# Kernel optimization log

Measured on AMD Instinct MI355X. Metric: run time of the kernel, lower is better.

The kernel has to match this reference:

```python
import jax, jax.numpy as jnp
import numpy as np
from jax.ops import segment_sum

N_NODES = 10000
N_EDGES = 160000
IN_FEAT = 256
OUT_FEAT = 256
NUM_RELS = 16


def setup_inputs() -> dict:
    key = jax.random.key(0)
    ks = jax.random.split(key, 8)
    feat = jax.random.normal(ks[0], (N_NODES, IN_FEAT), dtype=jnp.float32)
    Wf = jax.random.normal(ks[1], (NUM_RELS, IN_FEAT, OUT_FEAT), dtype=jnp.float32)
    Wb = jax.random.normal(ks[2], (NUM_RELS, IN_FEAT, OUT_FEAT), dtype=jnp.float32)
    loop_weight = jax.random.normal(ks[3], (IN_FEAT, OUT_FEAT), dtype=jnp.float32)
    forward_bias = jnp.zeros((OUT_FEAT,), dtype=jnp.float32)
    backward_bias = jnp.zeros((OUT_FEAT,), dtype=jnp.float32)
    self_bias = jnp.zeros((OUT_FEAT,), dtype=jnp.float32)
    src = jax.random.randint(ks[4], (N_EDGES,), 0, N_NODES, dtype=jnp.int32)
    dst = jax.random.randint(ks[5], (N_EDGES,), 0, N_NODES, dtype=jnp.int32)
    etypes = jax.random.randint(ks[6], (N_EDGES,), 0, NUM_RELS, dtype=jnp.int32)
    return {
        "feat": feat, "Wf": Wf, "Wb": Wb, "loop_weight": loop_weight,
        "forward_bias": forward_bias, "backward_bias": backward_bias,
        "self_bias": self_bias, "src": src, "dst": dst, "etypes": etypes,
        "use_dis_weight": 0, "drop_out": 0,
    }


def _inv_degree(idx, n):
    # dgl.norm_by_dst: 1/in-degree, with inf (zero-degree) replaced by 0
    deg = segment_sum(jnp.ones(idx.shape[0], dtype=jnp.float32), idx, num_segments=n)
    return jnp.where(deg > 0, 1.0 / deg, 0.0)


def _typed_pass(feat, W, bias, src_idx, dst_idx, etypes, norm_per_edge, n):
    # Per-relation projection of all nodes (grouped GEMM as R dense GEMMs),
    # then gather per-edge by (etype, src) -- avoids [E,in,out] weight gather.
    proj = jnp.einsum('ni,rio->rno', feat, W)          # [R, N, out]
    m = proj[etypes, src_idx] + bias                   # [E, out]
    m = m * norm_per_edge[:, None]
    return segment_sum(m, dst_idx, num_segments=n)     # [N, out]


def reference(feat, Wf, Wb, loop_weight, forward_bias, backward_bias,
              self_bias, src, dst, etypes, use_dis_weight, drop_out):
    n = feat.shape[0]
    # forward graph: messages src -> dst, norm by dst in-degree
    norm_f = _inv_degree(dst, n)[dst]                  # [E]
    m_forward = _typed_pass(feat, Wf, forward_bias, src, dst, etypes, norm_f, n)
    # reversed graph: src'=dst, dst'=src, same etype; norm by reversed dst in-degree
    norm_b = _inv_degree(src, n)[src]                  # [E]
    m_backward = _typed_pass(feat, Wb, backward_bias, dst, src, etypes, norm_b, n)
    # self loop (drop_out=False); faithful quirk: s += s + self_bias -> 2s + bias
    s = feat @ loop_weight
    s = s + s + self_bias
    return s + m_forward + m_backward
```

## Files before the change

kernel.cpp:

```cpp
#include <hip/hip_runtime.h>
#include <hip/hip_bf16.h>
#include <stdint.h>

#define N_NODES 10000
#define N_EDGES 160000
#define FEAT    256
#define NRELS   16
#define BM      64
#define NCHUNK  32
#define GRIDX   40
#define KBYTES  512

typedef __attribute__((ext_vector_type(8))) short bf16x8;
typedef __attribute__((ext_vector_type(4))) float f32x4;

__device__ __forceinline__ unsigned short f2bf(float f) {
    union { float f; unsigned u; } v; v.f = f;
    unsigned u = v.u;
    u += 0x7FFFu + ((u >> 16) & 1u);
    return (unsigned short)(u >> 16);
}
__device__ __forceinline__ float bf2f(unsigned short u) {
    union { unsigned u; float f; } v; v.u = ((unsigned)u) << 16;
    return v.f;
}

__global__ __launch_bounds__(256) void k_prep(const float4* __restrict__ src4,
                                              ushort4* __restrict__ dst4, int n4,
                                              const int* __restrict__ src,
                                              const int* __restrict__ dst,
                                              int* degd, int* degs) {
    int i = blockIdx.x * 256 + threadIdx.x;
    if (i < n4) {
        float4 v = src4[i];
        ushort4 r;
        r.x = f2bf(v.x); r.y = f2bf(v.y); r.z = f2bf(v.z); r.w = f2bf(v.w);
        dst4[i] = r;
    }
    if (i < N_EDGES) {
        atomicAdd(&degd[dst[i]], 1);
        atomicAdd(&degs[src[i]], 1);
    }
}

__global__ __launch_bounds__(256) void k_wtall(const float* __restrict__ Wf,
                                               const float* __restrict__ Wb,
                                               const float* __restrict__ lw,
                                               unsigned short* __restrict__ wall,
                                               unsigned short* __restrict__ lwt) {
    __shared__ float tile[64][65];
    int z = blockIdx.z;
    const float* w;
    unsigned short* o;
    if (z < 16)      { w = Wf + (size_t)z * 65536;        o = wall + (size_t)(z * 2) * 65536; }
    else if (z < 32) { w = Wb + (size_t)(z - 16) * 65536; o = wall + (size_t)((z - 16) * 2 + 1) * 65536; }
    else             { w = lw;                            o = lwt; }
    int i0 = blockIdx.x * 64, o0 = blockIdx.y * 64;
    int t = threadIdx.x;
    int c = t & 63, q = t >> 6;
#pragma unroll
    for (int it = 0; it < 16; it++) {
        int i = it * 4 + q;
        tile[i][c] = w[(size_t)(i0 + i) * 256 + o0 + c];
    }
    __syncthreads();
#pragma unroll
    for (int it = 0; it < 16; it++) {
        int oo = it * 4 + q;
        o[(size_t)(o0 + oo) * 256 + i0 + c] = f2bf(tile[c][oo]);
    }
}

__global__ __launch_bounds__(1024) void k_scan(const int* __restrict__ degd,
                                               const int* __restrict__ degs,
                                               int* offf, int* offb,
                                               int* curf, int* curb,
                                               float* normf, float* normb) {
    __shared__ int sf[1024], sb[1024];
    int t = threadIdx.x;
    const int CH = (N_NODES + 1023) / 1024;
    int base = t * CH;
    int sumf = 0, sumb = 0;
    for (int i = 0; i < CH; i++) {
        int n = base + i;
        if (n < N_NODES) { sumf += degd[n]; sumb += degs[n]; }
    }
    sf[t] = sumf; sb[t] = sumb;
    __syncthreads();
    for (int d = 1; d < 1024; d <<= 1) {
        int vf = (t >= d) ? sf[t - d] : 0;
        int vb = (t >= d) ? sb[t - d] : 0;
        __syncthreads();
        sf[t] += vf; sb[t] += vb;
        __syncthreads();
    }
    int runf = t ? sf[t - 1] : 0;
    int runb = t ? sb[t - 1] : 0;
    for (int i = 0; i < CH; i++) {
        int n = base + i;
        if (n < N_NODES) {
            int df = degd[n], db = degs[n];
            offf[n] = runf; offb[n] = runb;
            curf[n] = runf; curb[n] = runb;
            normf[n] = df > 0 ? 1.f / (float)df : 0.f;
            normb[n] = db > 0 ? 1.f / (float)db : 0.f;
            runf += df; runb += db;
        }
    }
    if (t == 1023) { offf[N_NODES] = runf; offb[N_NODES] = runb; }
}

__global__ __launch_bounds__(256) void k_fill(const int* __restrict__ et,
                                              const int* __restrict__ src,
                                              const int* __restrict__ dst,
                                              int* curf, int* curb,
                                              int* csrf, int* csrb) {
    int e = blockIdx.x * 256 + threadIdx.x;
    if (e < N_EDGES) {
        int s = src[e], d = dst[e], r = et[e];
        csrf[atomicAdd(&curf[d], 1)] = (r * 2) * N_NODES + s;
        csrb[atomicAdd(&curb[s], 1)] = (r * 2 + 1) * N_NODES + d;
    }
}

__global__ __launch_bounds__(256) void k_proj(const unsigned short* __restrict__ featb,
                                              const unsigned short* __restrict__ wall,
                                              const unsigned short* __restrict__ lwt,
                                              const float* __restrict__ sbias,
                                              unsigned short* __restrict__ proj,
                                              float* __restrict__ out) {
    __shared__ __align__(16) char lds[BM * KBYTES];
    int rd = blockIdx.x;
    if (rd > NCHUNK) return;
    int m0 = blockIdx.y * BM;
    int t = threadIdx.x;
    int wave = t >> 6, lane = t & 63;
    int nb = wave * 64, lr = lane & 15, lg = lane >> 4;
    bool self = (rd == NCHUNK);
    const unsigned short* wr = self ? lwt : wall + (size_t)rd * 256 * FEAT;

    {
        int rl = t >> 5;
        int kb = (t & 31) << 4;
#pragma unroll
        for (int it = 0; it < 8; it++) {
            int row = it * 8 + rl;
            int gr = m0 + row; if (gr > N_NODES - 1) gr = N_NODES - 1;
            bf16x8 v = *(const bf16x8*)(featb + gr * FEAT + (kb >> 1));
            *(bf16x8*)(lds + row * KBYTES + (kb ^ ((row & 7) << 4))) = v;
        }
    }
    __syncthreads();

    f32x4 acc[4][4] = {};
    bf16x8 bcur[4], bnxt[4];
#pragma unroll
    for (int ni = 0; ni < 4; ni++)
        bcur[ni] = *(const bf16x8*)(wr + (nb + ni * 16 + lr) * FEAT + lg * 8);
#pragma unroll
    for (int k0 = 0; k0 < FEAT; k0 += 32) {
        if (k0 + 32 < FEAT) {
#pragma unroll
            for (int ni = 0; ni < 4; ni++)
                bnxt[ni] = *(const bf16x8*)(wr + (nb + ni * 16 + lr) * FEAT + k0 + 32 + lg * 8);
        }
        int kb = (k0 + lg * 8) * 2;
        bf16x8 a[4];
#pragma unroll
        for (int mi = 0; mi < 4; mi++) {
            int row = mi * 16 + lr;
            a[mi] = *(const bf16x8*)(lds + row * KBYTES + (kb ^ ((row & 7) << 4)));
        }
#pragma unroll
        for (int mi = 0; mi < 4; mi++)
#pragma unroll
            for (int ni = 0; ni < 4; ni++)
                acc[mi][ni] = __builtin_amdgcn_mfma_f32_16x16x32_bf16(a[mi], bcur[ni], acc[mi][ni], 0, 0, 0);
#pragma unroll
        for (int ni = 0; ni < 4; ni++) bcur[ni] = bnxt[ni];
    }

    if (self) {
        for (int mi = 0; mi < 4; mi++) {
#pragma unroll
            for (int j = 0; j < 4; j++) {
                int row = m0 + mi * 16 + lg * 4 + j;
                if (row < N_NODES) {
                    for (int ni = 0; ni < 4; ni++) {
                        int col = nb + ni * 16 + lr;
                        out[(size_t)row * FEAT + col] = 2.0f * acc[mi][ni][j] + sbias[col];
                    }
                }
            }
        }
        return;
    }

    __syncthreads();
    for (int mi = 0; mi < 4; mi++) {
#pragma unroll
        for (int j = 0; j < 4; j++) {
            int row = mi * 16 + lg * 4 + j;
            int sw = (row & 7) << 4;
            for (int ni = 0; ni < 4; ni++) {
                int cb = (nb + ni * 16 + lr) * 2;
                *(unsigned short*)(lds + row * KBYTES + (cb ^ sw)) = f2bf(acc[mi][ni][j]);
            }
        }
    }
    __syncthreads();

    {
        int rl = t >> 5;
        int kb = (t & 31) << 4;
#pragma unroll
        for (int it = 0; it < 8; it++) {
            int row = it * 8 + rl;
            int gr = m0 + row;
            if (gr < N_NODES)
                *(bf16x8*)(proj + ((size_t)rd * N_NODES + gr) * FEAT + (kb >> 1)) =
                    *(const bf16x8*)(lds + row * KBYTES + (kb ^ ((row & 7) << 4)));
        }
    }
}

__global__ __launch_bounds__(256) void k_reduce(const unsigned short* __restrict__ proj,
                                                const int* __restrict__ csrf,
                                                const int* __restrict__ csrb,
                                                const int* __restrict__ offf,
                                                const int* __restrict__ offb,
                                                const float* __restrict__ normf,
                                                const float* __restrict__ normb,
                                                const float* __restrict__ biasf,
                                                const float* __restrict__ biasb,
                                                float* __restrict__ out) {
    int node = blockIdx.x * 4 + (threadIdx.x >> 6);
    if (node >= N_NODES) return;
    int lane = threadIdx.x & 63;
    int half = lane >> 5;
    int li = lane & 31;

    float af[8] = {0,0,0,0,0,0,0,0};
    float ab[8] = {0,0,0,0,0,0,0,0};

    int b0 = offf[node], b1 = offf[node + 1];
#pragma unroll 4
    for (int s = b0 + half; s < b1; s += 2) {
        int c = csrf[s];
        bf16x8 m = *(const bf16x8*)(proj + (size_t)c * FEAT + li * 8);
#pragma unroll
        for (int k = 0; k < 8; k++) af[k] += bf2f((unsigned short)m[k]);
    }
    int c0 = offb[node], c1 = offb[node + 1];
#pragma unroll 4
    for (int s = c0 + half; s < c1; s += 2) {
        int c = csrb[s];
        bf16x8 m = *(const bf16x8*)(proj + (size_t)c * FEAT + li * 8);
#pragma unroll
        for (int k = 0; k < 8; k++) ab[k] += bf2f((unsigned short)m[k]);
    }

    float nf = normf[node], nbv = normb[node];
    float v[8];
#pragma unroll
    for (int k = 0; k < 8; k++) v[k] = nf * af[k] + nbv * ab[k];
#pragma unroll
    for (int k = 0; k < 8; k++) v[k] += __shfl_xor(v[k], 32);

    int col = li * 8 + half * 4;
    float4 bfv = *(const float4*)(biasf + col);
    float4 bbv = *(const float4*)(biasb + col);
    float fb = (b1 > b0) ? 1.f : 0.f;
    float bb = (c1 > c0) ? 1.f : 0.f;
    float4 o = *(float4*)(out + (size_t)node * FEAT + col);
    int k0 = half * 4;
    o.x += v[k0 + 0] + fb * bfv.x + bb * bbv.x;
    o.y += v[k0 + 1] + fb * bfv.y + bb * bbv.y;
    o.z += v[k0 + 2] + fb * bfv.z + bb * bbv.z;
    o.w += v[k0 + 3] + fb * bfv.w + bb * bbv.w;
    *(float4*)(out + (size_t)node * FEAT + col) = o;
}

extern "C" void kernel_launch(void* const* d_in, const int* in_sizes, int n_in,
                              void* d_out, int out_size, void* d_ws, size_t ws_size,
                              hipStream_t stream) {
    const float* feat  = (const float*)d_in[0];
    const float* Wf    = (const float*)d_in[1];
    const float* Wb    = (const float*)d_in[2];
    const float* lw    = (const float*)d_in[3];
    const float* fbias = (const float*)d_in[4];
    const float* bbias = (const float*)d_in[5];
    const float* sbias = (const float*)d_in[6];
    const int*   src   = (const int*)d_in[7];
    const int*   dst   = (const int*)d_in[8];
    const int*   et    = (const int*)d_in[9];
    float* out = (float*)d_out;

    char* ws = (char*)d_ws;
    size_t off = 0;
    auto alloc = [&](size_t bytes) { void* p = ws + off; off = (off + bytes + 255) & ~(size_t)255; return p; };

    int*   degd  = (int*)alloc(N_NODES * 4);
    int*   degs  = (int*)alloc(N_NODES * 4);
    size_t zero_bytes = off;
    int*   offf  = (int*)alloc((N_NODES + 1) * 4);
    int*   offb  = (int*)alloc((N_NODES + 1) * 4);
    int*   curf  = (int*)alloc(N_NODES * 4);
    int*   curb  = (int*)alloc(N_NODES * 4);
    float* normf = (float*)alloc(N_NODES * 4);
    float* normb = (float*)alloc(N_NODES * 4);
    int*   csrf  = (int*)alloc(N_EDGES * 4);
    int*   csrb  = (int*)alloc(N_EDGES * 4);
    unsigned short* featb = (unsigned short*)alloc((size_t)N_NODES * FEAT * 2);
    unsigned short* wall  = (unsigned short*)alloc((size_t)NCHUNK * 256 * FEAT * 2);
    unsigned short* lwt   = (unsigned short*)alloc((size_t)FEAT * FEAT * 2);
    unsigned short* proj  = (unsigned short*)alloc((size_t)NCHUNK * N_NODES * FEAT * 2);
    (void)ws_size;

    hipMemsetAsync(d_ws, 0, zero_bytes, stream);

    {
        int n4 = N_NODES * FEAT / 4;
        k_prep<<<(n4 + 255) / 256, 256, 0, stream>>>((const float4*)feat, (ushort4*)featb, n4,
                                                     src, dst, degd, degs);
    }
    {
        dim3 gw(4, 4, 33);
        k_wtall<<<gw, 256, 0, stream>>>(Wf, Wb, lw, wall, lwt);
    }
    k_scan<<<1, 1024, 0, stream>>>(degd, degs, offf, offb, curf, curb, normf, normb);
    k_fill<<<(N_EDGES + 255) / 256, 256, 0, stream>>>(et, src, dst, curf, curb, csrf, csrb);

    {
        dim3 grid(GRIDX, (N_NODES + BM - 1) / BM);
        k_proj<<<grid, 256, 0, stream>>>(featb, wall, lwt, sbias, proj, out);
    }

    k_reduce<<<(N_NODES + 3) / 4, 256, 0, stream>>>(proj, csrf, csrb, offf, offb,
                                                    normf, normb, fbias, bbias, out);
}
```

Measured before the change: 225.7 us.

## Replace single-block scan with atomic block offsets, move self-loop into reduce

Replaces the single-block 1024-thread prefix scan with a multi-block kernel that gets per-block base offsets from global atomics. CSR segments stay contiguous per node but are no longer ordered by node id. The self-loop projection now goes through the same bf16 projection path as a 33rd slab, so k_reduce writes out directly instead of doing a read-modify-write of fp32 out. The LDS swizzle pattern for the epilogue store is also changed to cut bank conflicts. The costs are an extra bf16 rounding on the self-loop term and an extra 5 MB projection slab that k_reduce must read.

```diff
diff --git a/kernel.cpp b/kernel.cpp
--- a/kernel.cpp
+++ b/kernel.cpp
@@ -7,7 +7,7 @@
 #define FEAT    256
 #define NRELS   16
 #define BM      64
-#define NCHUNK  32
+#define NPROJ   33
 #define GRIDX   40
 #define KBYTES  512
 
@@ -46,15 +46,14 @@
 __global__ __launch_bounds__(256) void k_wtall(const float* __restrict__ Wf,
                                                const float* __restrict__ Wb,
                                                const float* __restrict__ lw,
-                                               unsigned short* __restrict__ wall,
-                                               unsigned short* __restrict__ lwt) {
+                                               unsigned short* __restrict__ wall) {
     __shared__ float tile[64][65];
     int z = blockIdx.z;
     const float* w;
     unsigned short* o;
     if (z < 16)      { w = Wf + (size_t)z * 65536;        o = wall + (size_t)(z * 2) * 65536; }
     else if (z < 32) { w = Wb + (size_t)(z - 16) * 65536; o = wall + (size_t)((z - 16) * 2 + 1) * 65536; }
-    else             { w = lw;                            o = lwt; }
+    else             { w = lw;                            o = wall + (size_t)32 * 65536; }
     int i0 = blockIdx.x * 64, o0 = blockIdx.y * 64;
     int t = threadIdx.x;
     int c = t & 63, q = t >> 6;
@@ -71,43 +70,40 @@
     }
 }
 
-__global__ __launch_bounds__(1024) void k_scan(const int* __restrict__ degd,
-                                               const int* __restrict__ degs,
-                                               int* offf, int* offb,
-                                               int* curf, int* curb,
-                                               float* normf, float* normb) {
-    __shared__ int sf[1024], sb[1024];
+__global__ __launch_bounds__(256) void k_off(const int* __restrict__ degd,
+                                             const int* __restrict__ degs,
+                                             int* offf, int* offb,
+                                             int* curf, int* curb,
+                                             float* normf, float* normb,
+                                             int* gcnt) {
+    __shared__ int sf[256], sb[256];
+    __shared__ int basef, baseb;
     int t = threadIdx.x;
-    const int CH = (N_NODES + 1023) / 1024;
-    int base = t * CH;
-    int sumf = 0, sumb = 0;
-    for (int i = 0; i < CH; i++) {
-        int n = base + i;
-        if (n < N_NODES) { sumf += degd[n]; sumb += degs[n]; }
-    }
-    sf[t] = sumf; sb[t] = sumb;
-    __syncthreads();
-    for (int d = 1; d < 1024; d <<= 1) {
+    int n = blockIdx.x * 256 + t;
+    int df = (n < N_NODES) ? degd[n] : 0;
+    int db = (n < N_NODES) ? degs[n] : 0;
+    sf[t] = df; sb[t] = db;
+    __syncthreads();
+    for (int d = 1; d < 256; d <<= 1) {
         int vf = (t >= d) ? sf[t - d] : 0;
         int vb = (t >= d) ? sb[t - d] : 0;
         __syncthreads();
         sf[t] += vf; sb[t] += vb;
         __syncthreads();
     }
-    int runf = t ? sf[t - 1] : 0;
-    int runb = t ? sb[t - 1] : 0;
-    for (int i = 0; i < CH; i++) {
-        int n = base + i;
-        if (n < N_NODES) {
-            int df = degd[n], db = degs[n];
-            offf[n] = runf; offb[n] = runb;
-            curf[n] = runf; curb[n] = runb;
-            normf[n] = df > 0 ? 1.f / (float)df : 0.f;
-            normb[n] = db > 0 ? 1.f / (float)db : 0.f;
-            runf += df; runb += db;
-        }
-    }
-    if (t == 1023) { offf[N_NODES] = runf; offb[N_NODES] = runb; }
+    if (t == 255) {
+        basef = atomicAdd(&gcnt[0], sf[255]);
+        baseb = atomicAdd(&gcnt[1], sb[255]);
+    }
+    __syncthreads();
+    if (n < N_NODES) {
+        int ef = basef + sf[t] - df;
+        int eb = baseb + sb[t] - db;
+        offf[n] = ef; offb[n] = eb;
+        curf[n] = ef; curb[n] = eb;
+        normf[n] = df > 0 ? 1.f / (float)df : 0.f;
+        normb[n] = db > 0 ? 1.f / (float)db : 0.f;
+    }
 }
 
 __global__ __launch_bounds__(256) void k_fill(const int* __restrict__ et,
@@ -125,19 +121,15 @@
 
 __global__ __launch_bounds__(256) void k_proj(const unsigned short* __restrict__ featb,
                                               const unsigned short* __restrict__ wall,
-                                              const unsigned short* __restrict__ lwt,
-                                              const float* __restrict__ sbias,
-                                              unsigned short* __restrict__ proj,
-                                              float* __restrict__ out) {
+                                              unsigned short* __restrict__ proj) {
     __shared__ __align__(16) char lds[BM * KBYTES];
     int rd = blockIdx.x;
-    if (rd > NCHUNK) return;
+    if (rd >= NPROJ) return;
     int m0 = blockIdx.y * BM;
     int t = threadIdx.x;
     int wave = t >> 6, lane = t & 63;
     int nb = wave * 64, lr = lane & 15, lg = lane >> 4;
-    bool self = (rd == NCHUNK);
-    const unsigned short* wr = self ? lwt : wall + (size_t)rd * 256 * FEAT;
+    const unsigned short* wr = wall + (size_t)rd * 256 * FEAT;
 
     {
         int rl = t >> 5;
@@ -180,28 +172,12 @@
         for (int ni = 0; ni < 4; ni++) bcur[ni] = bnxt[ni];
     }
 
-    if (self) {
-        for (int mi = 0; mi < 4; mi++) {
-#pragma unroll
-            for (int j = 0; j < 4; j++) {
-                int row = m0 + mi * 16 + lg * 4 + j;
-                if (row < N_NODES) {
-                    for (int ni = 0; ni < 4; ni++) {
-                        int col = nb + ni * 16 + lr;
-                        out[(size_t)row * FEAT + col] = 2.0f * acc[mi][ni][j] + sbias[col];
-                    }
-                }
-            }
-        }
-        return;
-    }
-
     __syncthreads();
     for (int mi = 0; mi < 4; mi++) {
 #pragma unroll
         for (int j = 0; j < 4; j++) {
             int row = mi * 16 + lg * 4 + j;
-            int sw = (row & 7) << 4;
+            int sw = ((row >> 2) & 3) << 5;
             for (int ni = 0; ni < 4; ni++) {
                 int cb = (nb + ni * 16 + lr) * 2;
                 *(unsigned short*)(lds + row * KBYTES + (cb ^ sw)) = f2bf(acc[mi][ni][j]);
@@ -219,7 +195,7 @@
             int gr = m0 + row;
             if (gr < N_NODES)
                 *(bf16x8*)(proj + ((size_t)rd * N_NODES + gr) * FEAT + (kb >> 1)) =
-                    *(const bf16x8*)(lds + row * KBYTES + (kb ^ ((row & 7) << 4)));
+                    *(const bf16x8*)(lds + row * KBYTES + (kb ^ (((row >> 2) & 3) << 5)));
         }
     }
 }
@@ -229,10 +205,13 @@
                                                 const int* __restrict__ csrb,
                                                 const int* __restrict__ offf,
                                                 const int* __restrict__ offb,
+                                                const int* __restrict__ degd,
+                                                const int* __restrict__ degs,
                                                 const float* __restrict__ normf,
                                                 const float* __restrict__ normb,
                                                 const float* __restrict__ biasf,
                                                 const float* __restrict__ biasb,
+                                                const float* __restrict__ sbias,
                                                 float* __restrict__ out) {
     int node = blockIdx.x * 4 + (threadIdx.x >> 6);
     if (node >= N_NODES) return;
@@ -243,7 +222,8 @@
     float af[8] = {0,0,0,0,0,0,0,0};
     float ab[8] = {0,0,0,0,0,0,0,0};
 
-    int b0 = offf[node], b1 = offf[node + 1];
+    int b0 = offf[node], dfc = degd[node];
+    int b1 = b0 + dfc;
 #pragma unroll 4
     for (int s = b0 + half; s < b1; s += 2) {
         int c = csrf[s];
@@ -251,7 +231,8 @@
 #pragma unroll
         for (int k = 0; k < 8; k++) af[k] += bf2f((unsigned short)m[k]);
     }
-    int c0 = offb[node], c1 = offb[node + 1];
+    int c0 = offb[node], dbc = degs[node];
+    int c1 = c0 + dbc;
 #pragma unroll 4
     for (int s = c0 + half; s < c1; s += 2) {
         int c = csrb[s];
@@ -267,17 +248,20 @@
 #pragma unroll
     for (int k = 0; k < 8; k++) v[k] += __shfl_xor(v[k], 32);
 
+    bf16x8 sf = *(const bf16x8*)(proj + ((size_t)32 * N_NODES + node) * FEAT + li * 8);
+
     int col = li * 8 + half * 4;
     float4 bfv = *(const float4*)(biasf + col);
     float4 bbv = *(const float4*)(biasb + col);
-    float fb = (b1 > b0) ? 1.f : 0.f;
-    float bb = (c1 > c0) ? 1.f : 0.f;
-    float4 o = *(float4*)(out + (size_t)node * FEAT + col);
+    float4 sbv = *(const float4*)(sbias + col);
+    float fb = (dfc > 0) ? 1.f : 0.f;
+    float bb = (dbc > 0) ? 1.f : 0.f;
     int k0 = half * 4;
-    o.x += v[k0 + 0] + fb * bfv.x + bb * bbv.x;
-    o.y += v[k0 + 1] + fb * bfv.y + bb * bbv.y;
-    o.z += v[k0 + 2] + fb * bfv.z + bb * bbv.z;
-    o.w += v[k0 + 3] + fb * bfv.w + bb * bbv.w;
+    float4 o;
+    o.x = v[k0 + 0] + 2.f * bf2f((unsigned short)sf[k0 + 0]) + sbv.x + fb * bfv.x + bb * bbv.x;
+    o.y = v[k0 + 1] + 2.f * bf2f((unsigned short)sf[k0 + 1]) + sbv.y + fb * bfv.y + bb * bbv.y;
+    o.z = v[k0 + 2] + 2.f * bf2f((unsigned short)sf[k0 + 2]) + sbv.z + fb * bfv.z + bb * bbv.z;
+    o.w = v[k0 + 3] + 2.f * bf2f((unsigned short)sf[k0 + 3]) + sbv.w + fb * bfv.w + bb * bbv.w;
     *(float4*)(out + (size_t)node * FEAT + col) = o;
 }
 
@@ -302,9 +286,10 @@
 
     int*   degd  = (int*)alloc(N_NODES * 4);
     int*   degs  = (int*)alloc(N_NODES * 4);
+    int*   gcnt  = (int*)alloc(64);
     size_t zero_bytes = off;
-    int*   offf  = (int*)alloc((N_NODES + 1) * 4);
-    int*   offb  = (int*)alloc((N_NODES + 1) * 4);
+    int*   offf  = (int*)alloc(N_NODES * 4);
+    int*   offb  = (int*)alloc(N_NODES * 4);
     int*   curf  = (int*)alloc(N_NODES * 4);
     int*   curb  = (int*)alloc(N_NODES * 4);
     float* normf = (float*)alloc(N_NODES * 4);
@@ -312,9 +297,8 @@
     int*   csrf  = (int*)alloc(N_EDGES * 4);
     int*   csrb  = (int*)alloc(N_EDGES * 4);
     unsigned short* featb = (unsigned short*)alloc((size_t)N_NODES * FEAT * 2);
-    unsigned short* wall  = (unsigned short*)alloc((size_t)NCHUNK * 256 * FEAT * 2);
-    unsigned short* lwt   = (unsigned short*)alloc((size_t)FEAT * FEAT * 2);
-    unsigned short* proj  = (unsigned short*)alloc((size_t)NCHUNK * N_NODES * FEAT * 2);
+    unsigned short* wall  = (unsigned short*)alloc((size_t)NPROJ * 256 * FEAT * 2);
+    unsigned short* proj  = (unsigned short*)alloc((size_t)NPROJ * N_NODES * FEAT * 2);
     (void)ws_size;
 
     hipMemsetAsync(d_ws, 0, zero_bytes, stream);
@@ -326,16 +310,18 @@
     }
     {
         dim3 gw(4, 4, 33);
-        k_wtall<<<gw, 256, 0, stream>>>(Wf, Wb, lw, wall, lwt);
-    }
-    k_scan<<<1, 1024, 0, stream>>>(degd, degs, offf, offb, curf, curb, normf, normb);
+        k_wtall<<<gw, 256, 0, stream>>>(Wf, Wb, lw, wall);
+    }
+    k_off<<<(N_NODES + 255) / 256, 256, 0, stream>>>(degd, degs, offf, offb, curf, curb,
+                                                     normf, normb, gcnt);
     k_fill<<<(N_EDGES + 255) / 256, 256, 0, stream>>>(et, src, dst, curf, curb, csrf, csrb);
 
     {
         dim3 grid(GRIDX, (N_NODES + BM - 1) / BM);
-        k_proj<<<grid, 256, 0, stream>>>(featb, wall, lwt, sbias, proj, out);
+        k_proj<<<grid, 256, 0, stream>>>(featb, wall, proj);
     }
 
     k_reduce<<<(N_NODES + 3) / 4, 256, 0, stream>>>(proj, csrf, csrb, offf, offb,
-                                                    normf, normb, fbias, bbias, out);
-}
+                                                    degd, degs, normf, normb,
+                                                    fbias, bbias, sbias, out);
+}
```

Result: faster. 213.1 us (-5.6%).
